# Optimization experiments

Hardware: AMD Instinct MI355X
Metric: run time of the kernel (lower is better)

## Reference

```python
import jax, jax.numpy as jnp
import numpy as np

# --- CT geometry (stand-in for ctlib `options`): parallel-beam Radon transform ---
H = 256; W = 256          # image size
V = 192                   # number of projection views
D = 256                   # detector bins
S = 256                   # samples along each ray
_SQ2 = float(np.sqrt(2.0))
_ANG = jnp.asarray(np.linspace(0.0, np.pi, V, endpoint=False), jnp.float32)      # view angles
_DET = jnp.asarray(np.linspace(-_SQ2, _SQ2, D), jnp.float32)                      # detector coords (world units, image in [-1,1]^2)
_T   = jnp.asarray(np.linspace(-_SQ2, _SQ2, S), jnp.float32)                      # sample positions along ray
_DT  = jnp.float32(2.0 * _SQ2 / S)                                                # ray step length


def _bilerp(img, xp, yp):
    """Bilinear gather from img [H,W] at pixel coords xp,yp; zero outside."""
    x0 = jnp.floor(xp); y0 = jnp.floor(yp)
    ix0 = x0.astype(jnp.int32); iy0 = y0.astype(jnp.int32)
    fx = xp - x0; fy = yp - y0
    def gat(ix, iy):
        valid = (ix >= 0) & (ix < W) & (iy >= 0) & (iy < H)
        v = img[jnp.clip(iy, 0, H - 1), jnp.clip(ix, 0, W - 1)]
        return jnp.where(valid, v, jnp.float32(0.0))
    return (gat(ix0, iy0) * (1 - fx) * (1 - fy)
            + gat(ix0 + 1, iy0) * fx * (1 - fy)
            + gat(ix0, iy0 + 1) * (1 - fx) * fy
            + gat(ix0 + 1, iy0 + 1) * fx * fy)


def project2d(img):
    """Ray-driven forward projection: img [H,W] -> sinogram [V,D]."""
    cos = jnp.cos(_ANG)[:, None, None]; sin = jnp.sin(_ANG)[:, None, None]
    s = _DET[None, :, None]; t = _T[None, None, :]
    # world coords of sample points along each ray: [V,D,S]
    xw = -s * sin + t * cos
    yw = s * cos + t * sin
    # world [-1,1] -> pixel coords
    xp = (xw + 1.0) * (W / 2.0) - 0.5
    yp = (yw + 1.0) * (H / 2.0) - 0.5
    return _bilerp(img, xp, yp).sum(-1) * _DT


def backproject2d(sino):
    """Exact adjoint of project2d (ray-driven scatter): [V,D] -> [H,W]."""
    _, vjp_fn = jax.vjp(project2d, jnp.zeros((H, W), sino.dtype))
    return vjp_fn(sino)[0]


def setup_inputs() -> dict:
    key = jax.random.key(0)
    k1, k2, k3 = jax.random.split(key, 3)
    input_data = jax.random.normal(k1, (2, 1, H, W), jnp.float32)
    proj = jax.random.normal(k2, (2, 1, V, D), jnp.float32)
    weight = jax.random.uniform(k3, (1,), jnp.float32)
    return {"input_data": input_data, "proj": proj, "weight": weight}


def reference(input_data, proj, weight):
    B, C = input_data.shape[:2]
    imgs = input_data.reshape(B * C, H, W)
    sino = jax.vmap(project2d)(imgs).reshape(proj.shape)          # A x
    temp = sino - proj                                            # A x - p
    ir = jax.vmap(backproject2d)(temp.reshape(B * C, V, D)).reshape(input_data.shape)  # A^T (A x - p)
    return input_data - weight * ir
```

## Files before the change

### kernel.cpp

```cpp
#include <hip/hip_runtime.h>
#include <math.h>

#define HH 256
#define WW 256
#define VV 192
#define DD 256
#define SS 256

#define DSQ2      1.41421356237309504880
#define F_DT      ((float)(2.0 * DSQ2 / 256.0))
#define F_INV_DS  ((float)(255.0 / (2.0 * DSQ2)))
#define F_SIG     ((float)(256.0 * DSQ2 / 255.0))
#define F_RAD     ((float)(128.0 * DSQ2))

#define TPITCH 67
#define NSEG 16
#define NV (VV / NSEG)

static __device__ __forceinline__ float view_angle(int v) {
    return (float)((double)v * (3.14159265358979323846 / 192.0));
}

__global__ __launch_bounds__(256)
void fwd_tile_kernel(const float* __restrict__ img_all,
                     float* __restrict__ sacc) {
    __shared__ float tile[66 * TPITCH];
    const int tx = (blockIdx.x & 3) << 6;
    const int ty = (blockIdx.x >> 2) << 6;
    const int v  = blockIdx.y;
    const int b  = blockIdx.z;
    const int tid  = threadIdx.x;
    const int lane = tid & 63;
    const int wv   = tid >> 6;

    const float* __restrict__ img = img_all + (b << 16);

    for (int k = tid; k < 64 * 16; k += 256) {
        const int r  = k >> 4;
        const int c4 = (k & 15) << 2;
        const float4 val = *(const float4*)(img + ((ty + r) << 8) + tx + c4);
        float* dst = tile + (r + 1) * TPITCH + 1 + c4;
        dst[0] = val.x; dst[1] = val.y; dst[2] = val.z; dst[3] = val.w;
    }
    if (tid < 132) {
        const int r  = tid >> 1;
        const int cc = (tid & 1) ? 65 : 0;
        const int gx = tx - 1 + cc;
        const int gy = ty - 1 + r;
        float vv = 0.0f;
        if ((unsigned)gx < 256u && (unsigned)gy < 256u) vv = img[(gy << 8) + gx];
        tile[r * TPITCH + cc] = vv;
    }
    if (tid < 128) {
        const int cc = 1 + (tid & 63);
        const int r  = (tid >> 6) ? 65 : 0;
        const int gx = tx - 1 + cc;
        const int gy = ty - 1 + r;
        float vv = 0.0f;
        if ((unsigned)gx < 256u && (unsigned)gy < 256u) vv = img[(gy << 8) + gx];
        tile[r * TPITCH + cc] = vv;
    }

    float sn, cs;
    sincosf(view_angle(v), &sn, &cs);
    const float Xd = -sn * F_SIG, Yd = cs * F_SIG;
    const float Xt =  cs * F_SIG, Yt = sn * F_SIG;
    const float X0 = 127.5f - F_RAD * (cs - sn);
    const float Y0 = 127.5f - F_RAD * (cs + sn);

    const int lox = (tx == 0) ? -1 : 0;
    const int loy = (ty == 0) ? -1 : 0;
    const unsigned spanx = (unsigned)(64 - lox);
    const unsigned spany = (unsigned)(64 - loy);

    const float xwl = ((float)(tx + lox) + 0.5f) * (1.0f / 128.0f) - 1.0f;
    const float xwh = ((float)(tx + 64)  + 0.5f) * (1.0f / 128.0f) - 1.0f;
    const float ywl = ((float)(ty + loy) + 0.5f) * (1.0f / 128.0f) - 1.0f;
    const float ywh = ((float)(ty + 64)  + 0.5f) * (1.0f / 128.0f) - 1.0f;
    const float dA = -xwl * sn, dB = -xwh * sn;
    const float dC =  ywl * cs, dDq =  ywh * cs;
    const float tAq =  xwl * cs, tB =  xwh * cs;
    const float tC =  ywl * sn, tD =  ywh * sn;
    const float dcmin = 127.5f + (fminf(dA, dB) + fminf(dC, dDq)) * F_INV_DS;
    const float dcmax = 127.5f + (fmaxf(dA, dB) + fmaxf(dC, dDq)) * F_INV_DS;
    const float tcmin = 127.5f + (fminf(tAq, tB) + fminf(tC, tD)) * F_INV_DS;
    const float tcmax = 127.5f + (fmaxf(tAq, tB) + fmaxf(tC, tD)) * F_INV_DS;
    const int dlo = max(0, (int)ceilf(dcmin - 0.002f));
    const int dhi = min(255, (int)floorf(dcmax + 0.002f));
    const int tlo = max(0, (int)ceilf(tcmin - 0.002f));
    const int thi = min(255, (int)floorf(tcmax + 0.002f));

    __syncthreads();

    const int sbase = (b * VV + v) << 8;
    for (int dbase = dlo; dbase <= dhi; dbase += 64) {
        const int d = dbase + lane;
        float acc = 0.0f;
        float xc = fmaf((float)d, Xd, fmaf((float)(tlo + wv), Xt, X0)) - (float)tx + 1.0f;
        float yc = fmaf((float)d, Yd, fmaf((float)(tlo + wv), Yt, Y0)) - (float)ty + 1.0f;
        const float step_x = 4.0f * Xt, step_y = 4.0f * Yt;
#pragma unroll 2
        for (int t = tlo + wv; t <= thi; t += 4) {
            const float xf = floorf(xc);
            const float yf = floorf(yc);
            const int cx = (int)xf;
            const int cy = (int)yf;
            const float fx = xc - xf;
            const float fy = yc - yf;
            const bool ok = (((unsigned)(cx - 1 - lox) < spanx) &
                             ((unsigned)(cy - 1 - loy) < spany));
            const int cxc = min(max(cx, 0), 65);
            const int cyc = min(max(cy, 0), 64);
            const float* p = tile + cyc * TPITCH + cxc;
            const float v00 = p[0],      v10 = p[1];
            const float v01 = p[TPITCH], v11 = p[TPITCH + 1];
            const float top = fmaf(fx, v10 - v00, v00);
            const float bot = fmaf(fx, v11 - v01, v01);
            const float smp = fmaf(fy, bot - top, top);
            acc += ok ? smp : 0.0f;
            xc += step_x; yc += step_y;
        }
        if (acc != 0.0f && d <= dhi)
            atomicAdd(sacc + sbase + d, acc);
    }
}

__global__ __launch_bounds__(256, 8)
void bwd_partial_kernel(const float* __restrict__ sacc,
                        const float* __restrict__ proj,
                        float* __restrict__ ir) {
    __shared__ float s_t[NV * DD];
    __shared__ float4 s_g[NV];
    const int tid = threadIdx.x;
    const int v0 = blockIdx.y * NV;
    const int b  = (int)blockIdx.x >> 7;

    if (tid < NV) {
        float sn, cs;
        sincosf(view_angle(v0 + tid), &sn, &cs);
        s_g[tid] = make_float4(cs, sn, F_SIG * cs, F_SIG * sn);
    }
    {
        const int base = (b * VV + v0) << 8;
        const float4* s4 = (const float4*)(sacc + base);
        const float4* p4 = (const float4*)(proj + base);
#pragma unroll
        for (int k = 0; k < NV * (DD / 4) / 256; ++k) {
            const int i = tid + (k << 8);
            const float4 a = s4[i];
            const float4 p = p4[i];
            float4 r;
            r.x = fmaf(F_DT, a.x, -p.x);
            r.y = fmaf(F_DT, a.y, -p.y);
            r.z = fmaf(F_DT, a.z, -p.z);
            r.w = fmaf(F_DT, a.w, -p.w);
            ((float4*)s_t)[i] = r;
        }
    }
    __syncthreads();

    const int idx = ((int)blockIdx.x << 9) + tid;
    const int y0 = (idx >> 8) & 255;
    const int x  = idx & 255;
    const float xw  = (float)x  * (1.0f / 128.0f) + (0.5f / 128.0f - 1.0f);
    const float yw0 = (float)y0 * (1.0f / 128.0f) + (0.5f / 128.0f - 1.0f);
    const float yw1 = yw0 + (1.0f / 128.0f);

    float acc0 = 0.0f, acc1 = 0.0f;
#pragma unroll 2
    for (int vi = 0; vi < NV; ++vi) {
        const float4 g = s_g[vi];
        const float* __restrict__ row = s_t + (vi << 8);
#pragma unroll
        for (int p = 0; p < 2; ++p) {
            const float yw = p ? yw1 : yw0;
            const float sw = fmaf(-xw, g.y, yw * g.x);
            const float tw = fmaf( xw, g.x, yw * g.y);
            const float dc = fmaf(sw, F_INV_DS, 127.5f);
            const float tc = fmaf(tw, F_INV_DS, 127.5f);
            const float d0f = floorf(dc);
            const float t0f = floorf(tc);
            const int d0 = (int)d0f;
            const float fd = dc - d0f;
            const float ft = tc - t0f;

            const float dx00 = fmaf(g.z, -ft, g.w * fd);
            const float dyn  = fmaf(g.z,  fd, g.w * ft);
            const float dx01 = dx00 + g.z;
            const float dy01 = g.w - dyn;
            const float dx10 = dx00 - g.w;
            const float dy10 = g.z - dyn;
            const float dx11 = dx01 - g.w;
            const float dy11 = dy10 + g.w;

            const float w00 = fmaxf(0.0f, 1.0f - fabsf(dx00)) * fmaxf(0.0f, 1.0f - fabsf(dyn));
            const float w01 = fmaxf(0.0f, 1.0f - fabsf(dx01)) * fmaxf(0.0f, 1.0f - fabsf(dy01));
            const float w10 = fmaxf(0.0f, 1.0f - fabsf(dx10)) * fmaxf(0.0f, 1.0f - fabsf(dy10));
            const float w11 = fmaxf(0.0f, 1.0f - fabsf(dx11)) * fmaxf(0.0f, 1.0f - fabsf(dy11));

            const float rA = row[d0];
            const float rB = row[d0 + 1];
            if (p == 0) {
                acc0 = fmaf(w00 + w01, rA, acc0);
                acc0 = fmaf(w10 + w11, rB, acc0);
            } else {
                acc1 = fmaf(w00 + w01, rA, acc1);
                acc1 = fmaf(w10 + w11, rB, acc1);
            }
        }
    }

    atomicAdd(ir + idx, acc0);
    atomicAdd(ir + idx + 256, acc1);
}

__global__ __launch_bounds__(256)
void combine_kernel(const float* __restrict__ input,
                    const float* __restrict__ ir,
                    const float* __restrict__ weight,
                    float* __restrict__ out) {
    const int i = blockIdx.x * 256 + threadIdx.x;
    const float4 a = ((const float4*)ir)[i];
    const float4 v = ((const float4*)input)[i];
    const float c = -weight[0] * F_DT;
    ((float4*)out)[i] = make_float4(fmaf(c, a.x, v.x), fmaf(c, a.y, v.y),
                                    fmaf(c, a.z, v.z), fmaf(c, a.w, v.w));
}

extern "C" void kernel_launch(void* const* d_in, const int* in_sizes, int n_in,
                              void* d_out, int out_size, void* d_ws, size_t ws_size,
                              hipStream_t stream) {
    const float* input  = (const float*)d_in[0];
    const float* proj   = (const float*)d_in[1];
    const float* weight = (const float*)d_in[2];
    float* out  = (float*)d_out;

    const int nb = in_sizes[0] / (HH * WW);
    const int npix = nb * HH * WW;
    const int nsino = nb * VV * DD;
    float* sacc = (float*)d_ws;
    float* ir   = sacc + nsino;

    hipMemsetAsync(d_ws, 0, (size_t)(nsino + npix) * sizeof(float), stream);
    fwd_tile_kernel<<<dim3(16, VV, nb), 256, 0, stream>>>(input, sacc);
    bwd_partial_kernel<<<dim3(npix / 512, NSEG), 256, 0, stream>>>(sacc, proj, ir);
    combine_kernel<<<npix / 1024, 256, 0, stream>>>(input, ir, weight, out);
}
```

Before: 102.6 us.

## Fuse memset, projection, backprojection and combine into one cooperative persistent kernel

Replaces the memset and three kernel launches with a single cooperative kernel that uses grid-wide syncs between phases. The kernel zeroes the sinogram buffer and copies the input into the output, runs the forward projection over a block-strided list of (tile, view) work items, then runs the backprojection and adds the scaled result straight into the output with atomics. This removes launch gaps and the separate ir buffer and combine pass. In exchange it pays for grid syncs and persistent-loop bookkeeping, and the backprojection loses its 8-blocks-per-CU occupancy hint and now shares one LDS allocation across both phases.

```diff
diff --git a/kernel.cpp b/kernel.cpp
--- a/kernel.cpp
+++ b/kernel.cpp
@@ -1,11 +1,13 @@
 #include <hip/hip_runtime.h>
+#include <hip/hip_cooperative_groups.h>
 #include <math.h>
+
+namespace cg = cooperative_groups;
 
 #define HH 256
 #define WW 256
 #define VV 192
 #define DD 256
-#define SS 256
 
 #define DSQ2      1.41421356237309504880
 #define F_DT      ((float)(2.0 * DSQ2 / 256.0))
@@ -22,209 +24,237 @@
 }
 
 __global__ __launch_bounds__(256)
-void fwd_tile_kernel(const float* __restrict__ img_all,
-                     float* __restrict__ sacc) {
-    __shared__ float tile[66 * TPITCH];
-    const int tx = (blockIdx.x & 3) << 6;
-    const int ty = (blockIdx.x >> 2) << 6;
-    const int v  = blockIdx.y;
-    const int b  = blockIdx.z;
+void fused_kernel(const float* __restrict__ input,
+                  const float* __restrict__ proj,
+                  const float* __restrict__ weight,
+                  float* __restrict__ out,
+                  float* __restrict__ sacc,
+                  int nb)
+{
+    cg::grid_group grid = cg::this_grid();
+    __shared__ float lds[66 * TPITCH];
+    __shared__ float4 s_g[NV];
     const int tid  = threadIdx.x;
     const int lane = tid & 63;
     const int wv   = tid >> 6;
-
-    const float* __restrict__ img = img_all + (b << 16);
-
-    for (int k = tid; k < 64 * 16; k += 256) {
-        const int r  = k >> 4;
-        const int c4 = (k & 15) << 2;
-        const float4 val = *(const float4*)(img + ((ty + r) << 8) + tx + c4);
-        float* dst = tile + (r + 1) * TPITCH + 1 + c4;
-        dst[0] = val.x; dst[1] = val.y; dst[2] = val.z; dst[3] = val.w;
+    const int G    = gridDim.x;
+    const int bid  = blockIdx.x;
+
+    {
+        const int nsino4 = nb * VV * (DD / 4);
+        float4* s4 = (float4*)sacc;
+        for (int i = bid * 256 + tid; i < nsino4; i += G * 256)
+            s4[i] = make_float4(0.f, 0.f, 0.f, 0.f);
+        const int npix4 = nb * HH * (WW / 4);
+        const float4* in4 = (const float4*)input;
+        float4* o4 = (float4*)out;
+        for (int i = bid * 256 + tid; i < npix4; i += G * 256)
+            o4[i] = in4[i];
     }
-    if (tid < 132) {
-        const int r  = tid >> 1;
-        const int cc = (tid & 1) ? 65 : 0;
-        const int gx = tx - 1 + cc;
-        const int gy = ty - 1 + r;
-        float vv = 0.0f;
-        if ((unsigned)gx < 256u && (unsigned)gy < 256u) vv = img[(gy << 8) + gx];
-        tile[r * TPITCH + cc] = vv;
-    }
-    if (tid < 128) {
-        const int cc = 1 + (tid & 63);
-        const int r  = (tid >> 6) ? 65 : 0;
-        const int gx = tx - 1 + cc;
-        const int gy = ty - 1 + r;
-        float vv = 0.0f;
-        if ((unsigned)gx < 256u && (unsigned)gy < 256u) vv = img[(gy << 8) + gx];
-        tile[r * TPITCH + cc] = vv;
-    }
-
-    float sn, cs;
-    sincosf(view_angle(v), &sn, &cs);
-    const float Xd = -sn * F_SIG, Yd = cs * F_SIG;
-    const float Xt =  cs * F_SIG, Yt = sn * F_SIG;
-    const float X0 = 127.5f - F_RAD * (cs - sn);
-    const float Y0 = 127.5f - F_RAD * (cs + sn);
-
-    const int lox = (tx == 0) ? -1 : 0;
-    const int loy = (ty == 0) ? -1 : 0;
-    const unsigned spanx = (unsigned)(64 - lox);
-    const unsigned spany = (unsigned)(64 - loy);
-
-    const float xwl = ((float)(tx + lox) + 0.5f) * (1.0f / 128.0f) - 1.0f;
-    const float xwh = ((float)(tx + 64)  + 0.5f) * (1.0f / 128.0f) - 1.0f;
-    const float ywl = ((float)(ty + loy) + 0.5f) * (1.0f / 128.0f) - 1.0f;
-    const float ywh = ((float)(ty + 64)  + 0.5f) * (1.0f / 128.0f) - 1.0f;
-    const float dA = -xwl * sn, dB = -xwh * sn;
-    const float dC =  ywl * cs, dDq =  ywh * cs;
-    const float tAq =  xwl * cs, tB =  xwh * cs;
-    const float tC =  ywl * sn, tD =  ywh * sn;
-    const float dcmin = 127.5f + (fminf(dA, dB) + fminf(dC, dDq)) * F_INV_DS;
-    const float dcmax = 127.5f + (fmaxf(dA, dB) + fmaxf(dC, dDq)) * F_INV_DS;
-    const float tcmin = 127.5f + (fminf(tAq, tB) + fminf(tC, tD)) * F_INV_DS;
-    const float tcmax = 127.5f + (fmaxf(tAq, tB) + fmaxf(tC, tD)) * F_INV_DS;
-    const int dlo = max(0, (int)ceilf(dcmin - 0.002f));
-    const int dhi = min(255, (int)floorf(dcmax + 0.002f));
-    const int tlo = max(0, (int)ceilf(tcmin - 0.002f));
-    const int thi = min(255, (int)floorf(tcmax + 0.002f));
-
-    __syncthreads();
-
-    const int sbase = (b * VV + v) << 8;
-    for (int dbase = dlo; dbase <= dhi; dbase += 64) {
-        const int d = dbase + lane;
-        float acc = 0.0f;
-        float xc = fmaf((float)d, Xd, fmaf((float)(tlo + wv), Xt, X0)) - (float)tx + 1.0f;
-        float yc = fmaf((float)d, Yd, fmaf((float)(tlo + wv), Yt, Y0)) - (float)ty + 1.0f;
-        const float step_x = 4.0f * Xt, step_y = 4.0f * Yt;
+    grid.sync();
+
+    {
+        const int N1 = nb * 16 * VV;
+        const int u0 = (int)((long long)bid * N1 / G);
+        const int u1 = (int)((long long)(bid + 1) * N1 / G);
+        int tg_cur = -1;
+        int tx = 0, ty = 0, b = 0, lox = 0, loy = 0;
+        unsigned spanx = 0, spany = 0;
+        float xwl = 0.f, xwh = 0.f, ywl = 0.f, ywh = 0.f;
+        for (int u = u0; u < u1; ++u) {
+            const int tg = u / VV;
+            const int v  = u - tg * VV;
+            if (tg != tg_cur) {
+                __syncthreads();
+                tg_cur = tg;
+                b  = tg >> 4;
+                tx = (tg & 3) << 6;
+                ty = ((tg >> 2) & 3) << 6;
+                const float* __restrict__ img = input + (b << 16);
+                for (int k = tid; k < 64 * 16; k += 256) {
+                    const int r  = k >> 4;
+                    const int c4 = (k & 15) << 2;
+                    const float4 val = *(const float4*)(img + ((ty + r) << 8) + tx + c4);
+                    float* dst = lds + (r + 1) * TPITCH + 1 + c4;
+                    dst[0] = val.x; dst[1] = val.y; dst[2] = val.z; dst[3] = val.w;
+                }
+                if (tid < 132) {
+                    const int r  = tid >> 1;
+                    const int cc = (tid & 1) ? 65 : 0;
+                    const int gx = tx - 1 + cc, gy = ty - 1 + r;
+                    float hv = 0.0f;
+                    if ((unsigned)gx < 256u && (unsigned)gy < 256u) hv = img[(gy << 8) + gx];
+                    lds[r * TPITCH + cc] = hv;
+                }
+                if (tid < 128) {
+                    const int cc = 1 + (tid & 63);
+                    const int r  = (tid >> 6) ? 65 : 0;
+                    const int gx = tx - 1 + cc, gy = ty - 1 + r;
+                    float hv = 0.0f;
+                    if ((unsigned)gx < 256u && (unsigned)gy < 256u) hv = img[(gy << 8) + gx];
+                    lds[r * TPITCH + cc] = hv;
+                }
+                lox = (tx == 0) ? -1 : 0;
+                loy = (ty == 0) ? -1 : 0;
+                spanx = (unsigned)(64 - lox);
+                spany = (unsigned)(64 - loy);
+                xwl = ((float)(tx + lox) + 0.5f) * (1.0f / 128.0f) - 1.0f;
+                xwh = ((float)(tx + 64)  + 0.5f) * (1.0f / 128.0f) - 1.0f;
+                ywl = ((float)(ty + loy) + 0.5f) * (1.0f / 128.0f) - 1.0f;
+                ywh = ((float)(ty + 64)  + 0.5f) * (1.0f / 128.0f) - 1.0f;
+                __syncthreads();
+            }
+
+            float sn, cs;
+            sincosf(view_angle(v), &sn, &cs);
+            const float Xd = -sn * F_SIG, Yd = cs * F_SIG;
+            const float Xt =  cs * F_SIG, Yt = sn * F_SIG;
+            const float X0 = 127.5f - F_RAD * (cs - sn);
+            const float Y0 = 127.5f - F_RAD * (cs + sn);
+
+            const float dA = -xwl * sn, dB = -xwh * sn;
+            const float dC =  ywl * cs, dDq =  ywh * cs;
+            const float tAq =  xwl * cs, tB =  xwh * cs;
+            const float tC =  ywl * sn, tD =  ywh * sn;
+            const float dcmin = 127.5f + (fminf(dA, dB) + fminf(dC, dDq)) * F_INV_DS;
+            const float dcmax = 127.5f + (fmaxf(dA, dB) + fmaxf(dC, dDq)) * F_INV_DS;
+            const float tcmin = 127.5f + (fminf(tAq, tB) + fminf(tC, tD)) * F_INV_DS;
+            const float tcmax = 127.5f + (fmaxf(tAq, tB) + fmaxf(tC, tD)) * F_INV_DS;
+            const int dlo = max(0, (int)ceilf(dcmin - 0.002f));
+            const int dhi = min(255, (int)floorf(dcmax + 0.002f));
+            const int tlo = max(0, (int)ceilf(tcmin - 0.002f));
+            const int thi = min(255, (int)floorf(tcmax + 0.002f));
+
+            const int sbase = (b * VV + v) << 8;
+            for (int dbase = dlo; dbase <= dhi; dbase += 64) {
+                const int d = dbase + lane;
+                float acc = 0.0f;
+                float xc = fmaf((float)d, Xd, fmaf((float)(tlo + wv), Xt, X0)) - (float)tx + 1.0f;
+                float yc = fmaf((float)d, Yd, fmaf((float)(tlo + wv), Yt, Y0)) - (float)ty + 1.0f;
+                const float step_x = 4.0f * Xt, step_y = 4.0f * Yt;
 #pragma unroll 2
-        for (int t = tlo + wv; t <= thi; t += 4) {
-            const float xf = floorf(xc);
-            const float yf = floorf(yc);
-            const int cx = (int)xf;
-            const int cy = (int)yf;
-            const float fx = xc - xf;
-            const float fy = yc - yf;
-            const bool ok = (((unsigned)(cx - 1 - lox) < spanx) &
-                             ((unsigned)(cy - 1 - loy) < spany));
-            const int cxc = min(max(cx, 0), 65);
-            const int cyc = min(max(cy, 0), 64);
-            const float* p = tile + cyc * TPITCH + cxc;
-            const float v00 = p[0],      v10 = p[1];
-            const float v01 = p[TPITCH], v11 = p[TPITCH + 1];
-            const float top = fmaf(fx, v10 - v00, v00);
-            const float bot = fmaf(fx, v11 - v01, v01);
-            const float smp = fmaf(fy, bot - top, top);
-            acc += ok ? smp : 0.0f;
-            xc += step_x; yc += step_y;
-        }
-        if (acc != 0.0f && d <= dhi)
-            atomicAdd(sacc + sbase + d, acc);
-    }
-}
-
-__global__ __launch_bounds__(256, 8)
-void bwd_partial_kernel(const float* __restrict__ sacc,
-                        const float* __restrict__ proj,
-                        float* __restrict__ ir) {
-    __shared__ float s_t[NV * DD];
-    __shared__ float4 s_g[NV];
-    const int tid = threadIdx.x;
-    const int v0 = blockIdx.y * NV;
-    const int b  = (int)blockIdx.x >> 7;
-
-    if (tid < NV) {
-        float sn, cs;
-        sincosf(view_angle(v0 + tid), &sn, &cs);
-        s_g[tid] = make_float4(cs, sn, F_SIG * cs, F_SIG * sn);
-    }
-    {
-        const int base = (b * VV + v0) << 8;
-        const float4* s4 = (const float4*)(sacc + base);
-        const float4* p4 = (const float4*)(proj + base);
-#pragma unroll
-        for (int k = 0; k < NV * (DD / 4) / 256; ++k) {
-            const int i = tid + (k << 8);
-            const float4 a = s4[i];
-            const float4 p = p4[i];
-            float4 r;
-            r.x = fmaf(F_DT, a.x, -p.x);
-            r.y = fmaf(F_DT, a.y, -p.y);
-            r.z = fmaf(F_DT, a.z, -p.z);
-            r.w = fmaf(F_DT, a.w, -p.w);
-            ((float4*)s_t)[i] = r;
+                for (int t = tlo + wv; t <= thi; t += 4) {
+                    const float xf = floorf(xc);
+                    const float yf = floorf(yc);
+                    const int cx = (int)xf;
+                    const int cy = (int)yf;
+                    const float fx = xc - xf;
+                    const float fy = yc - yf;
+                    const bool ok = (((unsigned)(cx - 1 - lox) < spanx) &
+                                     ((unsigned)(cy - 1 - loy) < spany));
+                    const int cxc = min(max(cx, 0), 65);
+                    const int cyc = min(max(cy, 0), 64);
+                    const float* p = lds + cyc * TPITCH + cxc;
+                    const float v00 = p[0],      v10 = p[1];
+                    const float v01 = p[TPITCH], v11 = p[TPITCH + 1];
+                    const float top = fmaf(fx, v10 - v00, v00);
+                    const float bot = fmaf(fx, v11 - v01, v01);
+                    const float smp = fmaf(fy, bot - top, top);
+                    acc += ok ? smp : 0.0f;
+                    xc += step_x; yc += step_y;
+                }
+                if (acc != 0.0f && d <= dhi)
+                    atomicAdd(sacc + sbase + d, acc);
+            }
         }
     }
-    __syncthreads();
-
-    const int idx = ((int)blockIdx.x << 9) + tid;
-    const int y0 = (idx >> 8) & 255;
-    const int x  = idx & 255;
-    const float xw  = (float)x  * (1.0f / 128.0f) + (0.5f / 128.0f - 1.0f);
-    const float yw0 = (float)y0 * (1.0f / 128.0f) + (0.5f / 128.0f - 1.0f);
-    const float yw1 = yw0 + (1.0f / 128.0f);
-
-    float acc0 = 0.0f, acc1 = 0.0f;
+    grid.sync();
+
+    {
+        const int N2 = (nb * HH * WW / 512) * NSEG;
+        const int u0 = (int)((long long)bid * N2 / G);
+        const int u1 = (int)((long long)(bid + 1) * N2 / G);
+        const float c = -weight[0] * F_DT;
+        int pb_cur = -1, idx = 0, b = 0;
+        float acc0 = 0.f, acc1 = 0.f, xw = 0.f, yw0 = 0.f, yw1 = 0.f;
+        for (int u = u0; u < u1; ++u) {
+            const int pb  = u >> 4;
+            const int seg = u & 15;
+            if (pb != pb_cur) {
+                if (pb_cur >= 0) {
+                    atomicAdd(out + idx, c * acc0);
+                    atomicAdd(out + idx + 256, c * acc1);
+                }
+                pb_cur = pb;
+                acc0 = acc1 = 0.f;
+                idx = (pb << 9) + tid;
+                b = pb >> 7;
+                const int y0 = (idx >> 8) & 255;
+                const int x  = idx & 255;
+                xw  = (float)x  * (1.0f / 128.0f) + (0.5f / 128.0f - 1.0f);
+                yw0 = (float)y0 * (1.0f / 128.0f) + (0.5f / 128.0f - 1.0f);
+                yw1 = yw0 + (1.0f / 128.0f);
+            }
+            __syncthreads();
+            if (tid < NV) {
+                float sn2, cs2;
+                sincosf(view_angle(seg * NV + tid), &sn2, &cs2);
+                s_g[tid] = make_float4(cs2, sn2, F_SIG * cs2, F_SIG * sn2);
+            }
+            {
+                const int base = (b * VV + seg * NV) << 8;
+                const float4* s4 = (const float4*)(sacc + base);
+                const float4* p4 = (const float4*)(proj + base);
+#pragma unroll
+                for (int k = 0; k < 3; ++k) {
+                    const int i = tid + (k << 8);
+                    const float4 a = s4[i];
+                    const float4 p = p4[i];
+                    ((float4*)lds)[i] = make_float4(
+                        fmaf(F_DT, a.x, -p.x), fmaf(F_DT, a.y, -p.y),
+                        fmaf(F_DT, a.z, -p.z), fmaf(F_DT, a.w, -p.w));
+                }
+            }
+            __syncthreads();
+
 #pragma unroll 2
-    for (int vi = 0; vi < NV; ++vi) {
-        const float4 g = s_g[vi];
-        const float* __restrict__ row = s_t + (vi << 8);
+            for (int vi = 0; vi < NV; ++vi) {
+                const float4 g = s_g[vi];
+                const float* __restrict__ row = lds + (vi << 8);
 #pragma unroll
-        for (int p = 0; p < 2; ++p) {
-            const float yw = p ? yw1 : yw0;
-            const float sw = fmaf(-xw, g.y, yw * g.x);
-            const float tw = fmaf( xw, g.x, yw * g.y);
-            const float dc = fmaf(sw, F_INV_DS, 127.5f);
-            const float tc = fmaf(tw, F_INV_DS, 127.5f);
-            const float d0f = floorf(dc);
-            const float t0f = floorf(tc);
-            const int d0 = (int)d0f;
-            const float fd = dc - d0f;
-            const float ft = tc - t0f;
-
-            const float dx00 = fmaf(g.z, -ft, g.w * fd);
-            const float dyn  = fmaf(g.z,  fd, g.w * ft);
-            const float dx01 = dx00 + g.z;
-            const float dy01 = g.w - dyn;
-            const float dx10 = dx00 - g.w;
-            const float dy10 = g.z - dyn;
-            const float dx11 = dx01 - g.w;
-            const float dy11 = dy10 + g.w;
-
-            const float w00 = fmaxf(0.0f, 1.0f - fabsf(dx00)) * fmaxf(0.0f, 1.0f - fabsf(dyn));
-            const float w01 = fmaxf(0.0f, 1.0f - fabsf(dx01)) * fmaxf(0.0f, 1.0f - fabsf(dy01));
-            const float w10 = fmaxf(0.0f, 1.0f - fabsf(dx10)) * fmaxf(0.0f, 1.0f - fabsf(dy10));
-            const float w11 = fmaxf(0.0f, 1.0f - fabsf(dx11)) * fmaxf(0.0f, 1.0f - fabsf(dy11));
-
-            const float rA = row[d0];
-            const float rB = row[d0 + 1];
-            if (p == 0) {
-                acc0 = fmaf(w00 + w01, rA, acc0);
-                acc0 = fmaf(w10 + w11, rB, acc0);
-            } else {
-                acc1 = fmaf(w00 + w01, rA, acc1);
-                acc1 = fmaf(w10 + w11, rB, acc1);
-            }
+                for (int p = 0; p < 2; ++p) {
+                    const float yw = p ? yw1 : yw0;
+                    const float sw = fmaf(-xw, g.y, yw * g.x);
+                    const float tw = fmaf( xw, g.x, yw * g.y);
+                    const float dc = fmaf(sw, F_INV_DS, 127.5f);
+                    const float tc = fmaf(tw, F_INV_DS, 127.5f);
+                    const float d0f = floorf(dc);
+                    const float t0f = floorf(tc);
+                    const int d0 = (int)d0f;
+                    const float fd = dc - d0f;
+                    const float ft = tc - t0f;
+
+                    const float dx00 = fmaf(g.z, -ft, g.w * fd);
+                    const float dyn  = fmaf(g.z,  fd, g.w * ft);
+                    const float dx01 = dx00 + g.z;
+                    const float dy01 = g.w - dyn;
+                    const float dx10 = dx00 - g.w;
+                    const float dy10 = g.z - dyn;
+                    const float dx11 = dx01 - g.w;
+                    const float dy11 = dy10 + g.w;
+
+                    const float w00 = fmaxf(0.0f, 1.0f - fabsf(dx00)) * fmaxf(0.0f, 1.0f - fabsf(dyn));
+                    const float w01 = fmaxf(0.0f, 1.0f - fabsf(dx01)) * fmaxf(0.0f, 1.0f - fabsf(dy01));
+                    const float w10 = fmaxf(0.0f, 1.0f - fabsf(dx10)) * fmaxf(0.0f, 1.0f - fabsf(dy10));
+                    const float w11 = fmaxf(0.0f, 1.0f - fabsf(dx11)) * fmaxf(0.0f, 1.0f - fabsf(dy11));
+
+                    const float rA = row[d0];
+                    const float rB = row[d0 + 1];
+                    if (p == 0) {
+                        acc0 = fmaf(w00 + w01, rA, acc0);
+                        acc0 = fmaf(w10 + w11, rB, acc0);
+                    } else {
+                        acc1 = fmaf(w00 + w01, rA, acc1);
+                        acc1 = fmaf(w10 + w11, rB, acc1);
+                    }
+                }
+            }
+        }
+        if (pb_cur >= 0) {
+            atomicAdd(out + idx, c * acc0);
+            atomicAdd(out + idx + 256, c * acc1);
         }
     }
-
-    atomicAdd(ir + idx, acc0);
-    atomicAdd(ir + idx + 256, acc1);
-}
-
-__global__ __launch_bounds__(256)
-void combine_kernel(const float* __restrict__ input,
-                    const float* __restrict__ ir,
-                    const float* __restrict__ weight,
-                    float* __restrict__ out) {
-    const int i = blockIdx.x * 256 + threadIdx.x;
-    const float4 a = ((const float4*)ir)[i];
-    const float4 v = ((const float4*)input)[i];
-    const float c = -weight[0] * F_DT;
-    ((float4*)out)[i] = make_float4(fmaf(c, a.x, v.x), fmaf(c, a.y, v.y),
-                                    fmaf(c, a.z, v.z), fmaf(c, a.w, v.w));
 }
 
 extern "C" void kernel_launch(void* const* d_in, const int* in_sizes, int n_in,
@@ -234,15 +264,17 @@
     const float* proj   = (const float*)d_in[1];
     const float* weight = (const float*)d_in[2];
     float* out  = (float*)d_out;
-
-    const int nb = in_sizes[0] / (HH * WW);
-    const int npix = nb * HH * WW;
-    const int nsino = nb * VV * DD;
     float* sacc = (float*)d_ws;
-    float* ir   = sacc + nsino;
-
-    hipMemsetAsync(d_ws, 0, (size_t)(nsino + npix) * sizeof(float), stream);
-    fwd_tile_kernel<<<dim3(16, VV, nb), 256, 0, stream>>>(input, sacc);
-    bwd_partial_kernel<<<dim3(npix / 512, NSEG), 256, 0, stream>>>(sacc, proj, ir);
-    combine_kernel<<<npix / 1024, 256, 0, stream>>>(input, ir, weight, out);
+    int nb = in_sizes[0] / (HH * WW);
+
+    int blocksPerCU = 0;
+    (void)hipOccupancyMaxActiveBlocksPerMultiprocessor(&blocksPerCU, fused_kernel, 256, 0);
+    if (blocksPerCU < 1) blocksPerCU = 1;
+    if (blocksPerCU > 8) blocksPerCU = 8;
+    int G = blocksPerCU * 256;
+    if (G > 2048) G = 2048;
+
+    void* args[] = { (void*)&input, (void*)&proj, (void*)&weight,
+                     (void*)&out, (void*)&sacc, (void*)&nb };
+    (void)hipLaunchCooperativeKernel(fused_kernel, dim3(G), dim3(256), args, 0, stream);
 }
```

New measurement: 237.4 us. +131.3%, slower.
